# Kernel tuning notes

Hardware: AMD Instinct MI355X
Metric: run time of the kernel (lower is better)

The kernel has to match this reference:

```python
import jax, jax.numpy as jnp
import numpy as np

D = 1024   # feature_dim
K = 10     # num_anchors
B = 16384  # batch
H = 8      # num_heads


def setup_inputs() -> dict:
    key = jax.random.key(0)
    ks = jax.random.split(key, 12)
    f32 = jnp.float32

    def w(k, shape, scale=0.02):
        return (jax.random.normal(k, shape, f32) * scale)

    return {
        "features": jax.random.normal(ks[0], (B, D), f32),
        "anchors": w(ks[1], (K, D), 0.1),
        # anchor_refiner: Linear(D, D//2) -> ReLU -> Linear(D//2, D) -> Tanh
        "ar_w1": w(ks[2], (D, D // 2)), "ar_b1": jnp.zeros((D // 2,), f32),
        "ar_w2": w(ks[3], (D // 2, D)), "ar_b2": jnp.zeros((D,), f32),
        # attention projections
        "q_w": w(ks[4], (D, D)), "q_b": jnp.zeros((D,), f32),
        "k_w": w(ks[5], (D, D)), "k_b": jnp.zeros((D,), f32),
        "v_w": w(ks[6], (D, D)), "v_b": jnp.zeros((D,), f32),
        "o_w": w(ks[7], (D, D)), "o_b": jnp.zeros((D,), f32),
        # feature_enhancer: LayerNorm -> Linear(D,2D) -> GELU -> Linear(2D,D)
        "ln_g": jnp.ones((D,), f32), "ln_b": jnp.zeros((D,), f32),
        "ff_w1": w(ks[8], (D, 2 * D)), "ff_b1": jnp.zeros((2 * D,), f32),
        "ff_w2": w(ks[9], (2 * D, D)), "ff_b2": jnp.zeros((D,), f32),
        "div_w": jnp.asarray(0.001, f32),
        "cen_w": jnp.asarray(0.001, f32),
    }


def _l2norm(x, eps=1e-8):
    n = jnp.linalg.norm(x, axis=-1, keepdims=True)
    return x / jnp.maximum(n, eps)


def _layernorm(x, g, b, eps=1e-5):
    mu = jnp.mean(x, axis=-1, keepdims=True)
    var = jnp.mean(jnp.square(x - mu), axis=-1, keepdims=True)
    return (x - mu) * jax.lax.rsqrt(var + eps) * g + b


def reference(features, anchors, ar_w1, ar_b1, ar_w2, ar_b2,
              q_w, q_b, k_w, k_b, v_w, v_b, o_w, o_b,
              ln_g, ln_b, ff_w1, ff_b1, ff_w2, ff_b2, div_w, cen_w):
    b = features.shape[0]
    hd = D // H
    fn = _l2norm(features)                                 # [B, D]

    # anchor refinement
    refin = jnp.tanh(jax.nn.relu(anchors @ ar_w1 + ar_b1) @ ar_w2 + ar_b2)
    an = _l2norm(anchors + 0.1 * refin)                    # [K, D]

    # multi-head cross-attention to anchors
    q = (fn @ q_w + q_b).reshape(b, H, hd)                 # [B, H, hd]
    k = (an @ k_w + k_b).reshape(K, H, hd)                 # [K, H, hd]
    v = (an @ v_w + v_b).reshape(K, H, hd)
    scores = jnp.einsum('bhd,khd->bhk', q, k) / jnp.sqrt(jnp.asarray(hd, fn.dtype))
    aw = jax.nn.softmax(scores, axis=-1)                   # [B, H, K]
    att = jnp.einsum('bhk,khd->bhd', aw, v).reshape(b, D)
    att = att @ o_w + o_b

    # feature enhancer (dropout inactive: eval mode)
    enh = fn + 0.1 * att
    h = jax.nn.gelu(_layernorm(enh, ln_g, ln_b) @ ff_w1 + ff_b1, approximate=False)
    enh = h @ ff_w2 + ff_b2
    final = fn + 0.2 * enh                                 # [B, D]

    # diversity loss: pdist over K=10 anchors (45 pairs)
    diff = an[:, None, :] - an[None, :, :]                 # [K, K, D]
    dmat = jnp.sqrt(jnp.maximum(jnp.sum(diff * diff, -1), 1e-24))
    iu = np.triu_indices(K, 1)
    div_loss = jnp.exp(-jnp.maximum(dmat[iu].mean(), 1e-6))

    # center loss: attention-weighted feature-anchor distances
    avg_att = aw.mean(axis=1)                              # [B, K]
    sq = (jnp.sum(fn * fn, 1, keepdims=True) + jnp.sum(an * an, 1)
          - 2.0 * fn @ an.T)
    fa_dist = jnp.sqrt(jnp.maximum(sq, 1e-12))             # [B, K]
    center_loss = jnp.sum(avg_att * fa_dist, axis=1).mean()

    geo = jnp.abs(div_w) * div_loss + jnp.abs(cen_w) * center_loss
    geo = jnp.clip(geo, 0.0, 0.01)
    return final, geo
```

## Files before the change

kernel.cpp:

```cpp
#include <hip/hip_runtime.h>
#include <hip/hip_bf16.h>
#include <math.h>

typedef __hip_bfloat16 bf16;

#define D_  1024
#define K_  10
#define B_  16384
#define H_  8
#define HD_ 128

struct alignas(16) BF8 { bf16 v[8]; };
struct alignas(8)  BF4 { bf16 v[4]; };

typedef __bf16 bf8v __attribute__((ext_vector_type(8)));
typedef float  f4v  __attribute__((ext_vector_type(4)));

__device__ __forceinline__ float b2f(bf16 x){ return __bfloat162float(x); }
__device__ __forceinline__ bf16  f2b(float x){ return __float2bfloat16(x); }

#define GL2LDS16(g, l) __builtin_amdgcn_global_load_lds( \
    (__attribute__((address_space(1))) void*)(g), \
    (__attribute__((address_space(3))) void*)(l), 16, 0, 0)

__global__ __launch_bounds__(256) void l2norm_k(const float* __restrict__ x,
                                                bf16* __restrict__ fnb) {
  int b = blockIdx.x, t = threadIdx.x;
  float4 v = ((const float4*)(x + (size_t)b * D_))[t];
  float p = v.x*v.x + v.y*v.y + v.z*v.z + v.w*v.w;
  #pragma unroll
  for (int o = 32; o > 0; o >>= 1) p += __shfl_down(p, o);
  __shared__ float wsum[4];
  if ((t & 63) == 0) wsum[t >> 6] = p;
  __syncthreads();
  __shared__ float inv_s;
  if (t == 0) inv_s = 1.f / fmaxf(sqrtf(wsum[0]+wsum[1]+wsum[2]+wsum[3]), 1e-8f);
  __syncthreads();
  float iv = inv_s;
  BF4 o;
  o.v[0] = f2b(v.x*iv); o.v[1] = f2b(v.y*iv);
  o.v[2] = f2b(v.z*iv); o.v[3] = f2b(v.w*iv);
  ((BF4*)(fnb + (size_t)b * D_))[t] = o;
}

__global__ __launch_bounds__(256) void wt_k(const float* __restrict__ w,
                                            bf16* __restrict__ wt, int R, int C) {
  __shared__ float tle[32][33];
  int c0 = blockIdx.x * 32, r0 = blockIdx.y * 32;
  int tx = threadIdx.x & 31, ty = threadIdx.x >> 5;
  #pragma unroll
  for (int i = 0; i < 32; i += 8)
    tle[ty + i][tx] = w[(size_t)(r0 + ty + i) * C + c0 + tx];
  __syncthreads();
  #pragma unroll
  for (int i = 0; i < 32; i += 8)
    wt[(size_t)(c0 + ty + i) * R + r0 + tx] = f2b(tle[tx][ty + i]);
}

template<int COLS, int KD, int ACT>
__global__ __launch_bounds__(256) void panelmm_k(
    const float* __restrict__ A, const float* __restrict__ W,
    const float* __restrict__ bias, const float* __restrict__ aux,
    float* __restrict__ out,
    const float* __restrict__ W2, const float* __restrict__ bias2,
    float* __restrict__ out2, int N, int npanel) {
  constexpr int GROUPS = 256 / COLS;
  constexpr int DCH = KD / GROUPS;
  __shared__ float A_s[K_][KD];
  __shared__ float part[K_][COLS][GROUPS];
  const int t = threadIdx.x;
  int blk = blockIdx.x;
  const float* Wm = W; const float* bm = bias; float* om = out;
  if (blk >= npanel) { blk -= npanel; Wm = W2; bm = bias2; om = out2; }
  const int panel = blk;
  for (int i = t; i < K_*KD; i += 256) A_s[0][i] = A[i];
  __syncthreads();
  const int cg = t % COLS, g = t / COLS;
  const int col = panel*COLS + cg;
  float s[K_];
  #pragma unroll
  for (int r = 0; r < K_; ++r) s[r] = 0.f;
  const float* wp = Wm + (size_t)(g*DCH)*N + col;
  for (int d = g*DCH; d < (g+1)*DCH; ++d) {
    float wv = *wp; wp += N;
    #pragma unroll
    for (int r = 0; r < K_; ++r) s[r] = fmaf(A_s[r][d], wv, s[r]);
  }
  #pragma unroll
  for (int r = 0; r < K_; ++r) part[r][cg][g] = s[r];
  __syncthreads();
  for (int o = t; o < K_*COLS; o += 256) {
    int r = o / COLS, c = o % COLS;
    float v = 0.f;
    #pragma unroll
    for (int gg = 0; gg < GROUPS; ++gg) v += part[r][c][gg];
    v += bm[panel*COLS + c];
    if constexpr (ACT == 1) v = fmaxf(v, 0.f);
    if constexpr (ACT == 2) v = aux[(size_t)r*N + panel*COLS + c] + 0.1f*tanhf(v);
    om[(size_t)r*N + panel*COLS + c] = v;
  }
}

template<int TRANSOUT, typename TW>
__global__ __launch_bounds__(256) void smallmm_k(
    const float* __restrict__ A, const TW* __restrict__ W,
    bf16* __restrict__ outb, float scale) {
  constexpr int COLS = 64, GROUPS = 4, DCH = 32, NW = 1024;
  __shared__ float A_s[K_][128];
  __shared__ float part[K_][COLS][GROUPS];
  const int t = threadIdx.x;
  const int h = blockIdx.x & 7, panel = blockIdx.x >> 3;
  for (int i = t; i < K_*128; i += 256) {
    int r = i >> 7, j = i & 127;
    A_s[r][j] = A[r*1024 + h*128 + j];
  }
  __syncthreads();
  const int cg = t % COLS, g = t / COLS;
  const int col = panel*COLS + cg;
  float s[K_];
  #pragma unroll
  for (int r = 0; r < K_; ++r) s[r] = 0.f;
  const TW* wp = W + (size_t)(h*128 + g*DCH)*NW + col;
  for (int d = g*DCH; d < g*DCH + DCH; ++d) {
    float wv;
    if constexpr (sizeof(TW) == 2) wv = b2f(*wp); else wv = *wp;
    wp += NW;
    #pragma unroll
    for (int r = 0; r < K_; ++r) s[r] = fmaf(A_s[r][d], wv, s[r]);
  }
  #pragma unroll
  for (int r = 0; r < K_; ++r) part[r][cg][g] = s[r];
  __syncthreads();
  for (int o = t; o < 16*COLS; o += 256) {
    int r = o / COLS, c = o % COLS;
    float v = 0.f;
    if (r < K_) {
      #pragma unroll
      for (int gg = 0; gg < GROUPS; ++gg) v += part[r][c][gg];
      v *= scale;
    }
    if constexpr (TRANSOUT) outb[(size_t)(panel*COLS + c)*128 + h*16 + r] = f2b(v);
    else                    outb[(size_t)(h*16 + r)*NW + panel*COLS + c] = f2b(v);
  }
}

__global__ void sbias_k(const float* __restrict__ qb, const float* __restrict__ Km,
                        const float* __restrict__ na, float* __restrict__ sb) {
  int c = threadIdx.x;
  if (c < 128) {
    int h = c >> 4, k = c & 15;
    float s = 0.f;
    if (k < K_) {
      for (int j = 0; j < HD_; ++j)
        s = fmaf(qb[h*HD_ + j], Km[(size_t)k*D_ + h*HD_ + j], s);
    }
    sb[c] = s * 0.08838834764831845f;
  } else {
    int j = c - 128;
    sb[c] = (j < K_) ? (1.f + na[j]) : 0.f;
  }
}

__global__ __launch_bounds__(256) void anext_k(const float* __restrict__ an,
                                               bf16* __restrict__ wt) {
  int k = blockIdx.x;
  bf16* dst = wt + (size_t)(128 + k) * 1024;
  int i = threadIdx.x * 4;
  BF4 o;
  if (k < K_) {
    float4 a = *(const float4*)(an + (size_t)k*1024 + i);
    o.v[0] = f2b(-2.f*a.x); o.v[1] = f2b(-2.f*a.y);
    o.v[2] = f2b(-2.f*a.z); o.v[3] = f2b(-2.f*a.w);
  } else {
    o.v[0] = o.v[1] = o.v[2] = o.v[3] = f2b(0.f);
  }
  *(BF4*)(dst + i) = o;
}

__global__ __launch_bounds__(256) void ar3_k(const float* __restrict__ an_un,
    float* __restrict__ an, float* __restrict__ na, float* __restrict__ divloss) {
  __shared__ float a_s[K_][D_];
  __shared__ float nrm[K_];
  __shared__ float dm[45];
  const int t = threadIdx.x;
  for (int i = t; i < K_*D_; i += 256) a_s[0][i] = an_un[i];
  __syncthreads();
  const int wid = t >> 6, lane = t & 63;
  for (int r = wid; r < K_; r += 4) {
    float p = 0.f;
    for (int j = lane; j < D_; j += 64) p += a_s[r][j]*a_s[r][j];
    #pragma unroll
    for (int o = 1; o < 64; o <<= 1) p += __shfl_xor(p, o);
    if (lane == 0) nrm[r] = p;
  }
  __syncthreads();
  for (int i = t; i < K_*D_; i += 256) {
    int r = i >> 10;
    float iv = 1.f / fmaxf(sqrtf(nrm[r]), 1e-8f);
    float v = a_s[0][i] * iv;
    a_s[0][i] = v;
    an[i] = v;
  }
  if (t < K_) {
    float iv = 1.f / fmaxf(sqrtf(nrm[t]), 1e-8f);
    na[t] = nrm[t] * iv * iv;
  }
  __syncthreads();
  const int pr = t >> 2, sub = t & 3;
  if (pr < 45) {
    int i = 0, j = 0, c = pr;
    for (i = 0; i < K_; ++i) { int cnt = K_-1-i; if (c < cnt) { j = i+1+c; break; } c -= cnt; }
    float s = 0.f;
    for (int d = sub*256; d < sub*256 + 256; ++d) {
      float df = a_s[i][d] - a_s[j][d]; s += df*df;
    }
    s += __shfl_xor(s, 1); s += __shfl_xor(s, 2);
    if (sub == 0) dm[pr] = sqrtf(fmaxf(s, 1e-24f));
  }
  __syncthreads();
  if (t == 0) {
    float m = 0.f;
    for (int p = 0; p < 45; ++p) m += dm[p];
    m *= (1.f/45.f);
    *divloss = expf(-fmaxf(m, 1e-6f));
  }
}

template<int EPI, typename TO>
__global__ __launch_bounds__(256) void mgemm_k(
    const bf16* __restrict__ A, const bf16* __restrict__ Bt,
    const float* __restrict__ bias, const bf16* __restrict__ aux,
    TO* __restrict__ out, int M, int N, int Kd, float scale) {
  constexpr int BM = 128, BN = 128, BK = 32;
  __shared__ bf16 As[BM][BK];
  __shared__ bf16 Bs[BN][BK];
  const int tid = threadIdx.x;
  const int nMB = M / BM;
  const int nwg = gridDim.x;
  int wg = blockIdx.x;
  wg = (wg & 7) * (nwg >> 3) + (wg >> 3);
  const int mb = wg % nMB, nb = wg / nMB;
  const int bm = mb * BM, bn = nb * BN;

  const int srow = tid >> 2;
  const int sk   = (tid & 3) * 8;
  const bf16* ga = A  + (size_t)(bm + srow) * Kd + sk;
  const bf16* gb = Bt + (size_t)(bn + srow) * Kd + sk;
  const size_t rstep = (size_t)64 * Kd;
  bf16* la = &As[0][0] + tid * 8;
  bf16* lb = &Bs[0][0] + tid * 8;

  const int w    = tid >> 6;
  const int lane = tid & 63;
  const int wr = (w >> 1) * 64, wc = (w & 1) * 64;
  const int fr = lane & 15, fg = lane >> 4;

  f4v acc[4][4];
  const f4v zz = {0.f, 0.f, 0.f, 0.f};
  #pragma unroll
  for (int m = 0; m < 4; ++m)
    #pragma unroll
    for (int n = 0; n < 4; ++n) acc[m][n] = zz;

  for (int k0 = 0; k0 < Kd; k0 += BK) {
    GL2LDS16(ga,         la);
    GL2LDS16(ga + rstep, la + 2048);
    GL2LDS16(gb,         lb);
    GL2LDS16(gb + rstep, lb + 2048);
    __syncthreads();
    bf8v af[4], bf_[4];
    #pragma unroll
    for (int m = 0; m < 4; ++m)
      af[m] = *(const bf8v*)&As[wr + m*16 + fr][fg*8];
    #pragma unroll
    for (int n = 0; n < 4; ++n)
      bf_[n] = *(const bf8v*)&Bs[wc + n*16 + fr][fg*8];
    #pragma unroll
    for (int m = 0; m < 4; ++m)
      #pragma unroll
      for (int n = 0; n < 4; ++n)
        acc[m][n] = __builtin_amdgcn_mfma_f32_16x16x32_bf16(af[m], bf_[n], acc[m][n], 0, 0, 0);
    __syncthreads();
    ga += BK; gb += BK;
  }

  float bv[4];
  #pragma unroll
  for (int n = 0; n < 4; ++n) bv[n] = bias[bn + wc + n*16 + fr];
  #pragma unroll
  for (int m = 0; m < 4; ++m) {
    #pragma unroll
    for (int r = 0; r < 4; ++r) {
      const int row = bm + wr + m*16 + fg*4 + r;
      #pragma unroll
      for (int n = 0; n < 4; ++n) {
        const int col = bn + wc + n*16 + fr;
        float x = acc[m][n][r] + bv[n];
        if constexpr (EPI == 1) x = b2f(aux[(size_t)row * N + col]) + scale * x;
        if constexpr (EPI == 2) x = 0.5f * x * (1.f + erff(x * 0.70710678118654752f));
        if constexpr (sizeof(TO) == 2) out[(size_t)row * N + col] = f2b(x);
        else                           out[(size_t)row * N + col] = x;
      }
    }
  }
}

template<int EPI, typename TO>
__global__ __launch_bounds__(512) void mgemm256_k(
    const bf16* __restrict__ A, const bf16* __restrict__ Bt,
    const float* __restrict__ bias, const bf16* __restrict__ aux,
    TO* __restrict__ out, int M, int N, int Kd, float scale) {
  constexpr int BM = 256, BN = 256, BK = 64;
  __shared__ bf16 As[2][BM*BK];
  __shared__ bf16 Bs[2][BN*BK];
  const int tid = threadIdx.x;
  const int nMB = M / BM;
  const int nwg = gridDim.x;
  int wg = blockIdx.x;
  wg = (wg & 7) * (nwg >> 3) + (wg >> 3);
  const int bm = (wg % nMB) * BM, bn = (wg / nMB) * BN;

  const int srow = tid >> 3;
  const int scsw = ((tid & 7) ^ (srow & 7)) * 8;
  const bf16* gA = A  + (size_t)(bm + srow) * Kd + scsw;
  const bf16* gB = Bt + (size_t)(bn + srow) * Kd + scsw;
  const size_t lstep = (size_t)64 * Kd;

  const int wid = tid >> 6, lane = tid & 63;
  const int wm = wid >> 2, wn = wid & 3;
  const int fr = lane & 15, fg = lane >> 4;
  const int fsw = fr & 7;

  f4v acc[8][4];
  const f4v zz = {0.f, 0.f, 0.f, 0.f};
  #pragma unroll
  for (int m = 0; m < 8; ++m)
    #pragma unroll
    for (int n = 0; n < 4; ++n) acc[m][n] = zz;

  const int nt = Kd / BK;

  #pragma unroll
  for (int l = 0; l < 4; ++l) {
    GL2LDS16(gA + l*lstep, &As[0][0] + tid*8 + l*4096);
    GL2LDS16(gB + l*lstep, &Bs[0][0] + tid*8 + l*4096);
  }
  __syncthreads();

  int buf = 0;
  for (int t = 0; t < nt; ++t) {
    if (t + 1 < nt) {
      const int ko = (t + 1) * BK;
      #pragma unroll
      for (int l = 0; l < 4; ++l) {
        GL2LDS16(gA + l*lstep + ko, &As[buf^1][0] + tid*8 + l*4096);
        GL2LDS16(gB + l*lstep + ko, &Bs[buf^1][0] + tid*8 + l*4096);
      }
    }
    const bf16* la = &As[buf][0];
    const bf16* lb = &Bs[buf][0];
    bf8v bq[8];
    #pragma unroll
    for (int n = 0; n < 4; ++n) {
      const int rb = wn*64 + n*16 + fr;
      bq[n*2]   = *(const bf8v*)(lb + rb*64 + ((fg     ^ fsw) * 8));
      bq[n*2+1] = *(const bf8v*)(lb + rb*64 + (((4+fg) ^ fsw) * 8));
    }
    __builtin_amdgcn_s_setprio(1);
    #pragma unroll
    for (int m = 0; m < 8; ++m) {
      const int ra = wm*128 + m*16 + fr;
      bf8v a0 = *(const bf8v*)(la + ra*64 + ((fg     ^ fsw) * 8));
      bf8v a1 = *(const bf8v*)(la + ra*64 + (((4+fg) ^ fsw) * 8));
      #pragma unroll
      for (int n = 0; n < 4; ++n) {
        acc[m][n] = __builtin_amdgcn_mfma_f32_16x16x32_bf16(a0, bq[n*2],   acc[m][n], 0, 0, 0);
        acc[m][n] = __builtin_amdgcn_mfma_f32_16x16x32_bf16(a1, bq[n*2+1], acc[m][n], 0, 0, 0);
      }
    }
    __builtin_amdgcn_s_setprio(0);
    __syncthreads();
    buf ^= 1;
  }

  float bv[4];
  #pragma unroll
  for (int n = 0; n < 4; ++n) bv[n] = bias[bn + wn*64 + n*16 + fr];
  #pragma unroll
  for (int m = 0; m < 8; ++m) {
    #pragma unroll
    for (int r = 0; r < 4; ++r) {
      const int row = bm + wm*128 + m*16 + fg*4 + r;
      #pragma unroll
      for (int n = 0; n < 4; ++n) {
        const int col = bn + wn*64 + n*16 + fr;
        float x = acc[m][n][r] + bv[n];
        if constexpr (EPI == 1) x = b2f(aux[(size_t)row * N + col]) + scale * x;
        if constexpr (EPI == 2) x = 0.5f * x * (1.f + erff(x * 0.70710678118654752f));
        if constexpr (sizeof(TO) == 2) out[(size_t)row * N + col] = f2b(x);
        else                           out[(size_t)row * N + col] = x;
      }
    }
  }
}

__global__ __launch_bounds__(256) void attn2_k(
    const float* __restrict__ S, bf16* __restrict__ awp,
    float* __restrict__ cen_acc) {
  __shared__ float cred[4];
  const int t = threadIdx.x;
  const int wid = t >> 6, lane = t & 63;
  const int sub = lane & 7, head = lane >> 3;
  const int k0 = sub*2, k1 = k0 + 1;
  float c_acc = 0.f;
  const int row0 = blockIdx.x * 32 + wid * 8;

  for (int i = 0; i < 8; ++i) {
    const int row = row0 + i;
    const float* Sr = S + (size_t)row * 256;
    float2 sv = *(const float2*)(Sr + head*16 + k0);
    float v0 = (k0 < K_) ? sv.x : -1e30f;
    float v1 = (k1 < K_) ? sv.y : -1e30f;
    float m = fmaxf(v0, v1);
    m = fmaxf(m, __shfl_xor(m,1)); m = fmaxf(m, __shfl_xor(m,2)); m = fmaxf(m, __shfl_xor(m,4));
    float e0 = (k0 < K_) ? __expf(v0 - m) : 0.f;
    float e1 = (k1 < K_) ? __expf(v1 - m) : 0.f;
    float es = e0 + e1;
    es += __shfl_xor(es,1); es += __shfl_xor(es,2); es += __shfl_xor(es,4);
    float inv = 1.f / es;
    float a0 = e0 * inv, a1 = e1 * inv;
    bf16 b0 = f2b(a0), b1 = f2b(a1);
    unsigned int pk = (unsigned int)(*(unsigned short*)&b0)
                    | ((unsigned int)(*(unsigned short*)&b1) << 16);
    *(unsigned int*)(awp + (size_t)row*128 + head*16 + k0) = pk;
    float g0 = a0, g1 = a1;
    g0 += __shfl_xor(g0,8); g0 += __shfl_xor(g0,16); g0 += __shfl_xor(g0,32);
    g1 += __shfl_xor(g1,8); g1 += __shfl_xor(g1,16); g1 += __shfl_xor(g1,32);
    if (sub < 5) {
      float d20 = Sr[128 + k0];
      float d21 = Sr[128 + k1];
      c_acc = fmaf(g0, sqrtf(fmaxf(d20, 1e-12f)), c_acc);
      c_acc = fmaf(g1, sqrtf(fmaxf(d21, 1e-12f)), c_acc);
    }
  }
  #pragma unroll
  for (int o = 1; o < 64; o <<= 1) c_acc += __shfl_xor(c_acc, o);
  if (lane == 0) cred[wid] = c_acc;
  __syncthreads();
  if (t == 0) {
    float s = (cred[0]+cred[1]+cred[2]+cred[3]) * (1.f/64.f/(float)B_);
    atomicAdd(cen_acc, s);
  }
}

__global__ __launch_bounds__(256) void ln_k(const bf16* __restrict__ x,
    const float* __restrict__ g, const float* __restrict__ bta,
    bf16* __restrict__ out) {
  int b = blockIdx.x, t = threadIdx.x;
  BF4 ld = ((const BF4*)(x + (size_t)b * D_))[t];
  float v[4];
  #pragma unroll
  for (int j = 0; j < 4; ++j) v[j] = b2f(ld.v[j]);
  float s = v[0]+v[1]+v[2]+v[3];
  #pragma unroll
  for (int o = 32; o > 0; o >>= 1) s += __shfl_down(s, o);
  __shared__ float w1[4], w2[4];
  if ((t & 63) == 0) w1[t >> 6] = s;
  __syncthreads();
  __shared__ float mu_s, rs_s;
  if (t == 0) mu_s = (w1[0]+w1[1]+w1[2]+w1[3]) * (1.f/D_);
  __syncthreads();
  float mu = mu_s;
  float qv = 0.f;
  #pragma unroll
  for (int j = 0; j < 4; ++j) { float d = v[j]-mu; qv += d*d; }
  #pragma unroll
  for (int o = 32; o > 0; o >>= 1) qv += __shfl_down(qv, o);
  if ((t & 63) == 0) w2[t >> 6] = qv;
  __syncthreads();
  if (t == 0) rs_s = rsqrtf((w2[0]+w2[1]+w2[2]+w2[3]) * (1.f/D_) + 1e-5f);
  __syncthreads();
  float rs = rs_s;
  BF4 o;
  #pragma unroll
  for (int j = 0; j < 4; ++j) {
    int col = t*4 + j;
    o.v[j] = f2b((v[j]-mu)*rs*g[col] + bta[col]);
  }
  ((BF4*)(out + (size_t)b * D_))[t] = o;
}

__global__ void geo_k(const float* __restrict__ divl, const float* __restrict__ cen,
                      const float* __restrict__ div_w, const float* __restrict__ cen_w,
                      float* __restrict__ out) {
  float g = fabsf(*div_w) * (*divl) + fabsf(*cen_w) * (*cen);
  out[0] = fminf(fmaxf(g, 0.f), 0.01f);
}

extern "C" void kernel_launch(void* const* d_in, const int* in_sizes, int n_in,
                              void* d_out, int out_size, void* d_ws, size_t ws_size,
                              hipStream_t stream) {
  const float* features = (const float*)d_in[0];
  const float* anchors  = (const float*)d_in[1];
  const float* ar_w1 = (const float*)d_in[2];
  const float* ar_b1 = (const float*)d_in[3];
  const float* ar_w2 = (const float*)d_in[4];
  const float* ar_b2 = (const float*)d_in[5];
  const float* q_w = (const float*)d_in[6];
  const float* q_b = (const float*)d_in[7];
  const float* k_w = (const float*)d_in[8];
  const float* k_b = (const float*)d_in[9];
  const float* v_w = (const float*)d_in[10];
  const float* v_b = (const float*)d_in[11];
  const float* o_w = (const float*)d_in[12];
  const float* o_b = (const float*)d_in[13];
  const float* ln_g = (const float*)d_in[14];
  const float* ln_b = (const float*)d_in[15];
  const float* ff_w1 = (const float*)d_in[16];
  const float* ff_b1 = (const float*)d_in[17];
  const float* ff_w2 = (const float*)d_in[18];
  const float* ff_b2 = (const float*)d_in[19];
  const float* div_w = (const float*)d_in[20];
  const float* cen_w = (const float*)d_in[21];
  float* out = (float*)d_out;

  char* w = (char*)d_ws;
  bf16* ws_fnb = (bf16*)w;  w += (size_t)B_ * D_ * 2;
  bf16* ws_enh = (bf16*)w;  w += (size_t)B_ * D_ * 2;
  bf16* ws_ln  = (bf16*)w;  w += (size_t)B_ * D_ * 2;
  bf16* ws_h   = (bf16*)w;  w += (size_t)B_ * 2048 * 2;
  float* ws_S  = (float*)w; w += (size_t)B_ * 256 * 4;
  bf16* ws_awp = (bf16*)w;  w += (size_t)B_ * 128 * 2;
  bf16* ws_wq  = (bf16*)w;  w += (size_t)D_ * D_ * 2;
  bf16* ws_w1t = (bf16*)w;  w += (size_t)D_ * 2048 * 2;
  bf16* ws_w2t = (bf16*)w;  w += (size_t)2048 * D_ * 2;
  bf16* ws_wt  = (bf16*)w;  w += (size_t)256 * D_ * 2;
  bf16* ws_vt  = (bf16*)w;  w += (size_t)D_ * 128 * 2;
  float* ws_har = (float*)w;  w += (size_t)K_ * (D_/2) * 4;
  float* ws_anu = (float*)w;  w += (size_t)K_ * D_ * 4;
  float* ws_an  = (float*)w;  w += (size_t)K_ * D_ * 4;
  float* ws_k   = (float*)w;  w += (size_t)K_ * D_ * 4;
  float* ws_v   = (float*)w;  w += (size_t)K_ * D_ * 4;
  float* ws_na  = (float*)w;  w += 256;
  float* ws_div = (float*)w;  w += 256;
  float* ws_cen = (float*)w;  w += 256;
  float* ws_sb  = (float*)w;  w += 512;
  if ((size_t)(w - (char*)d_ws) > ws_size) return;

  hipMemsetAsync(ws_cen, 0, 4, stream);

  wt_k<<<dim3(D_/32,   D_/32),   256, 0, stream>>>(q_w,   ws_wq,  D_,   D_);
  wt_k<<<dim3(2048/32, D_/32),   256, 0, stream>>>(ff_w1, ws_w1t, D_,   2048);
  wt_k<<<dim3(D_/32,   2048/32), 256, 0, stream>>>(ff_w2, ws_w2t, 2048, D_);

  l2norm_k<<<B_, 256, 0, stream>>>(features, ws_fnb);

  panelmm_k<32, 1024, 1><<<16, 256, 0, stream>>>(
      anchors, ar_w1, ar_b1, nullptr, ws_har,
      nullptr, nullptr, nullptr, D_/2, 16);
  panelmm_k<64, 512, 2><<<16, 256, 0, stream>>>(
      ws_har, ar_w2, ar_b2, anchors, ws_anu,
      nullptr, nullptr, nullptr, D_, 16);
  ar3_k<<<1, 256, 0, stream>>>(ws_anu, ws_an, ws_na, ws_div);
  panelmm_k<64, 1024, 0><<<32, 256, 0, stream>>>(
      ws_an, k_w, k_b, nullptr, ws_k,
      v_w, v_b, ws_v, D_, 16);

  smallmm_k<0, bf16><<<128, 256, 0, stream>>>(ws_k, ws_wq, ws_wt, 0.08838834764831845f);
  anext_k<<<128, 256, 0, stream>>>(ws_an, ws_wt);
  sbias_k<<<1, 256, 0, stream>>>(q_b, ws_k, ws_na, ws_sb);
  smallmm_k<1, float><<<128, 256, 0, stream>>>(ws_v, o_w, ws_vt, 1.f);

  mgemm_k<0, float><<<dim3((B_/128)*(256/128)), 256, 0, stream>>>(
      ws_fnb, ws_wt, ws_sb, nullptr, ws_S, B_, 256, D_, 0.f);

  attn2_k<<<B_/32, 256, 0, stream>>>(ws_S, ws_awp, ws_cen);

  mgemm256_k<1, bf16><<<dim3((B_/256)*(D_/256)), 512, 0, stream>>>(
      ws_awp, ws_vt, o_b, ws_fnb, ws_enh, B_, D_, 128, 0.1f);

  ln_k<<<B_, 256, 0, stream>>>(ws_enh, ln_g, ln_b, ws_ln);

  mgemm256_k<2, bf16><<<dim3((B_/256)*(2048/256)), 512, 0, stream>>>(
      ws_ln, ws_w1t, ff_b1, nullptr, ws_h, B_, 2048, D_, 0.f);

  mgemm256_k<1, float><<<dim3((B_/256)*(D_/256)), 512, 0, stream>>>(
      ws_h, ws_w2t, ff_b2, ws_fnb, out, B_, D_, 2048, 0.2f);

  geo_k<<<1, 1, 0, stream>>>(ws_div, ws_cen, div_w, cen_w, out + (size_t)B_ * D_);
}
```

Baseline: 420.0 us.

## Double-buffer small GEMM, fuse prep/transpose launches, templatize K dims

Merges three weight-transpose launches into one kernel and four small prep kernels (K/V projection folding, anchor extension, score bias) into one multi-role kernel to cut launch overhead. Rewrites the 128x128 MFMA GEMM with double-buffered LDS, XOR-swizzled layout, and priority hints so global loads overlap compute. Makes K a compile-time template parameter for both GEMMs so loops can unroll. Switches the attention-output GEMM (K=128) from 256-tile to 128-tile to improve occupancy across CUs. These add code complexity and more LDS per block in the small GEMM.

```diff
diff --git a/kernel.cpp b/kernel.cpp
--- a/kernel.cpp
+++ b/kernel.cpp
@@ -43,10 +43,19 @@
   ((BF4*)(fnb + (size_t)b * D_))[t] = o;
 }
 
-__global__ __launch_bounds__(256) void wt_k(const float* __restrict__ w,
-                                            bf16* __restrict__ wt, int R, int C) {
+__global__ __launch_bounds__(256) void wt3_k(
+    const float* __restrict__ qw, const float* __restrict__ w1,
+    const float* __restrict__ w2,
+    bf16* __restrict__ o_qw, bf16* __restrict__ o_w1, bf16* __restrict__ o_w2) {
   __shared__ float tle[32][33];
-  int c0 = blockIdx.x * 32, r0 = blockIdx.y * 32;
+  int b = blockIdx.x;
+  const float* w; bf16* wt; int R, C, c0, r0;
+  if (b < 1024)      { w = qw; wt = o_qw; R = 1024; C = 1024;
+                       c0 = (b & 31) * 32;      r0 = (b >> 5) * 32; }
+  else if (b < 3072) { int i = b - 1024; w = w1; wt = o_w1; R = 1024; C = 2048;
+                       c0 = (i % 64) * 32;      r0 = (i / 64) * 32; }
+  else               { int i = b - 3072; w = w2; wt = o_w2; R = 2048; C = 1024;
+                       c0 = (i % 32) * 32;      r0 = (i / 32) * 32; }
   int tx = threadIdx.x & 31, ty = threadIdx.x >> 5;
   #pragma unroll
   for (int i = 0; i < 32; i += 8)
@@ -101,15 +110,63 @@
   }
 }
 
+__global__ __launch_bounds__(256) void ar3_k(const float* __restrict__ an_un,
+    float* __restrict__ an, float* __restrict__ na, float* __restrict__ divloss) {
+  __shared__ float a_s[K_][D_];
+  __shared__ float nrm[K_];
+  __shared__ float dm[45];
+  const int t = threadIdx.x;
+  for (int i = t; i < K_*D_; i += 256) a_s[0][i] = an_un[i];
+  __syncthreads();
+  const int wid = t >> 6, lane = t & 63;
+  for (int r = wid; r < K_; r += 4) {
+    float p = 0.f;
+    for (int j = lane; j < D_; j += 64) p += a_s[r][j]*a_s[r][j];
+    #pragma unroll
+    for (int o = 1; o < 64; o <<= 1) p += __shfl_xor(p, o);
+    if (lane == 0) nrm[r] = p;
+  }
+  __syncthreads();
+  for (int i = t; i < K_*D_; i += 256) {
+    int r = i >> 10;
+    float iv = 1.f / fmaxf(sqrtf(nrm[r]), 1e-8f);
+    float v = a_s[0][i] * iv;
+    a_s[0][i] = v;
+    an[i] = v;
+  }
+  if (t < K_) {
+    float iv = 1.f / fmaxf(sqrtf(nrm[t]), 1e-8f);
+    na[t] = nrm[t] * iv * iv;
+  }
+  __syncthreads();
+  const int pr = t >> 2, sub = t & 3;
+  if (pr < 45) {
+    int i = 0, j = 0, c = pr;
+    for (i = 0; i < K_; ++i) { int cnt = K_-1-i; if (c < cnt) { j = i+1+c; break; } c -= cnt; }
+    float s = 0.f;
+    for (int d = sub*256; d < sub*256 + 256; ++d) {
+      float df = a_s[i][d] - a_s[j][d]; s += df*df;
+    }
+    s += __shfl_xor(s, 1); s += __shfl_xor(s, 2);
+    if (sub == 0) dm[pr] = sqrtf(fmaxf(s, 1e-24f));
+  }
+  __syncthreads();
+  if (t == 0) {
+    float m = 0.f;
+    for (int p = 0; p < 45; ++p) m += dm[p];
+    m *= (1.f/45.f);
+    *divloss = expf(-fmaxf(m, 1e-6f));
+  }
+}
+
 template<int TRANSOUT, typename TW>
-__global__ __launch_bounds__(256) void smallmm_k(
-    const float* __restrict__ A, const TW* __restrict__ W,
-    bf16* __restrict__ outb, float scale) {
+__device__ __forceinline__ void smallmm_body(
+    int blk, const float* __restrict__ A, const TW* __restrict__ W,
+    bf16* __restrict__ outb, float scale,
+    float (&A_s)[K_][128], float (&part)[K_][64][4]) {
   constexpr int COLS = 64, GROUPS = 4, DCH = 32, NW = 1024;
-  __shared__ float A_s[K_][128];
-  __shared__ float part[K_][COLS][GROUPS];
   const int t = threadIdx.x;
-  const int h = blockIdx.x & 7, panel = blockIdx.x >> 3;
+  const int h = blk & 7, panel = blk >> 3;
   for (int i = t; i < K_*128; i += 256) {
     int r = i >> 7, j = i & 127;
     A_s[r][j] = A[r*1024 + h*128 + j];
@@ -121,12 +178,12 @@
   #pragma unroll
   for (int r = 0; r < K_; ++r) s[r] = 0.f;
   const TW* wp = W + (size_t)(h*128 + g*DCH)*NW + col;
-  for (int d = g*DCH; d < g*DCH + DCH; ++d) {
+  for (int d = 0; d < DCH; ++d) {
     float wv;
     if constexpr (sizeof(TW) == 2) wv = b2f(*wp); else wv = *wp;
     wp += NW;
     #pragma unroll
-    for (int r = 0; r < K_; ++r) s[r] = fmaf(A_s[r][d], wv, s[r]);
+    for (int r = 0; r < K_; ++r) s[r] = fmaf(A_s[r][g*DCH + d], wv, s[r]);
   }
   #pragma unroll
   for (int r = 0; r < K_; ++r) part[r][cg][g] = s[r];
@@ -144,116 +201,77 @@
   }
 }
 
-__global__ void sbias_k(const float* __restrict__ qb, const float* __restrict__ Km,
-                        const float* __restrict__ na, float* __restrict__ sb) {
-  int c = threadIdx.x;
-  if (c < 128) {
-    int h = c >> 4, k = c & 15;
-    float s = 0.f;
+__global__ __launch_bounds__(256) void prep_k(
+    const float* __restrict__ Km, const float* __restrict__ Vm,
+    const float* __restrict__ an, const float* __restrict__ na,
+    const bf16* __restrict__ wq, const float* __restrict__ ow,
+    const float* __restrict__ qb,
+    bf16* __restrict__ wt, bf16* __restrict__ vt, float* __restrict__ sb) {
+  __shared__ float A_s[K_][128];
+  __shared__ float part[K_][64][4];
+  const int b = blockIdx.x;
+  if (b < 128) {
+    smallmm_body<0, bf16>(b, Km, wq, wt, 0.08838834764831845f, A_s, part);
+  } else if (b < 256) {
+    smallmm_body<1, float>(b - 128, Vm, ow, vt, 1.f, A_s, part);
+  } else if (b < 384) {
+    int k = b - 256;
+    bf16* dst = wt + (size_t)(128 + k) * 1024;
+    int i = threadIdx.x * 4;
+    BF4 o;
     if (k < K_) {
-      for (int j = 0; j < HD_; ++j)
-        s = fmaf(qb[h*HD_ + j], Km[(size_t)k*D_ + h*HD_ + j], s);
-    }
-    sb[c] = s * 0.08838834764831845f;
+      float4 a = *(const float4*)(an + (size_t)k*1024 + i);
+      o.v[0] = f2b(-2.f*a.x); o.v[1] = f2b(-2.f*a.y);
+      o.v[2] = f2b(-2.f*a.z); o.v[3] = f2b(-2.f*a.w);
+    } else {
+      o.v[0] = o.v[1] = o.v[2] = o.v[3] = f2b(0.f);
+    }
+    *(BF4*)(dst + i) = o;
   } else {
-    int j = c - 128;
-    sb[c] = (j < K_) ? (1.f + na[j]) : 0.f;
-  }
-}
-
-__global__ __launch_bounds__(256) void anext_k(const float* __restrict__ an,
-                                               bf16* __restrict__ wt) {
-  int k = blockIdx.x;
-  bf16* dst = wt + (size_t)(128 + k) * 1024;
-  int i = threadIdx.x * 4;
-  BF4 o;
-  if (k < K_) {
-    float4 a = *(const float4*)(an + (size_t)k*1024 + i);
-    o.v[0] = f2b(-2.f*a.x); o.v[1] = f2b(-2.f*a.y);
-    o.v[2] = f2b(-2.f*a.z); o.v[3] = f2b(-2.f*a.w);
-  } else {
-    o.v[0] = o.v[1] = o.v[2] = o.v[3] = f2b(0.f);
-  }
-  *(BF4*)(dst + i) = o;
-}
-
-__global__ __launch_bounds__(256) void ar3_k(const float* __restrict__ an_un,
-    float* __restrict__ an, float* __restrict__ na, float* __restrict__ divloss) {
-  __shared__ float a_s[K_][D_];
-  __shared__ float nrm[K_];
-  __shared__ float dm[45];
-  const int t = threadIdx.x;
-  for (int i = t; i < K_*D_; i += 256) a_s[0][i] = an_un[i];
-  __syncthreads();
-  const int wid = t >> 6, lane = t & 63;
-  for (int r = wid; r < K_; r += 4) {
-    float p = 0.f;
-    for (int j = lane; j < D_; j += 64) p += a_s[r][j]*a_s[r][j];
-    #pragma unroll
-    for (int o = 1; o < 64; o <<= 1) p += __shfl_xor(p, o);
-    if (lane == 0) nrm[r] = p;
-  }
-  __syncthreads();
-  for (int i = t; i < K_*D_; i += 256) {
-    int r = i >> 10;
-    float iv = 1.f / fmaxf(sqrtf(nrm[r]), 1e-8f);
-    float v = a_s[0][i] * iv;
-    a_s[0][i] = v;
-    an[i] = v;
-  }
-  if (t < K_) {
-    float iv = 1.f / fmaxf(sqrtf(nrm[t]), 1e-8f);
-    na[t] = nrm[t] * iv * iv;
-  }
-  __syncthreads();
-  const int pr = t >> 2, sub = t & 3;
-  if (pr < 45) {
-    int i = 0, j = 0, c = pr;
-    for (i = 0; i < K_; ++i) { int cnt = K_-1-i; if (c < cnt) { j = i+1+c; break; } c -= cnt; }
-    float s = 0.f;
-    for (int d = sub*256; d < sub*256 + 256; ++d) {
-      float df = a_s[i][d] - a_s[j][d]; s += df*df;
-    }
-    s += __shfl_xor(s, 1); s += __shfl_xor(s, 2);
-    if (sub == 0) dm[pr] = sqrtf(fmaxf(s, 1e-24f));
-  }
-  __syncthreads();
-  if (t == 0) {
-    float m = 0.f;
-    for (int p = 0; p < 45; ++p) m += dm[p];
-    m *= (1.f/45.f);
-    *divloss = expf(-fmaxf(m, 1e-6f));
-  }
-}
-
-template<int EPI, typename TO>
+    int c = threadIdx.x;
+    if (c < 128) {
+      int h = c >> 4, k = c & 15;
+      float s = 0.f;
+      if (k < K_) {
+        for (int j = 0; j < HD_; ++j)
+          s = fmaf(qb[h*HD_ + j], Km[(size_t)k*D_ + h*HD_ + j], s);
+      }
+      sb[c] = s * 0.08838834764831845f;
+    } else {
+      int j = c - 128;
+      sb[c] = (j < K_) ? (1.f + na[j]) : 0.f;
+    }
+  }
+}
+
+template<int EPI, int KD, typename TO>
 __global__ __launch_bounds__(256) void mgemm_k(
     const bf16* __restrict__ A, const bf16* __restrict__ Bt,
     const float* __restrict__ bias, const bf16* __restrict__ aux,
-    TO* __restrict__ out, int M, int N, int Kd, float scale) {
+    TO* __restrict__ out, int M, int N, float scale) {
   constexpr int BM = 128, BN = 128, BK = 32;
-  __shared__ bf16 As[BM][BK];
-  __shared__ bf16 Bs[BN][BK];
+  constexpr int nt = KD / BK;
+  __shared__ bf16 As[2][BM*BK];
+  __shared__ bf16 Bs[2][BN*BK];
   const int tid = threadIdx.x;
   const int nMB = M / BM;
   const int nwg = gridDim.x;
   int wg = blockIdx.x;
   wg = (wg & 7) * (nwg >> 3) + (wg >> 3);
-  const int mb = wg % nMB, nb = wg / nMB;
-  const int bm = mb * BM, bn = nb * BN;
+  const int bm = (wg % nMB) * BM, bn = (wg / nMB) * BN;
 
   const int srow = tid >> 2;
-  const int sk   = (tid & 3) * 8;
-  const bf16* ga = A  + (size_t)(bm + srow) * Kd + sk;
-  const bf16* gb = Bt + (size_t)(bn + srow) * Kd + sk;
-  const size_t rstep = (size_t)64 * Kd;
-  bf16* la = &As[0][0] + tid * 8;
-  bf16* lb = &Bs[0][0] + tid * 8;
+  const int ssw  = (((tid & 3) ^ ((tid >> 3) & 3)) * 8);
+  const bf16* gA = A  + (size_t)(bm + srow) * KD + ssw;
+  const bf16* gB = Bt + (size_t)(bn + srow) * KD + ssw;
+  const size_t rstep = (size_t)64 * KD;
 
   const int w    = tid >> 6;
   const int lane = tid & 63;
   const int wr = (w >> 1) * 64, wc = (w & 1) * 64;
   const int fr = lane & 15, fg = lane >> 4;
+  const int key = (fr >> 1) & 3;
+  const int co  = (fg ^ key) * 8;
 
   f4v acc[4][4];
   const f4v zz = {0.f, 0.f, 0.f, 0.f};
@@ -262,26 +280,39 @@
     #pragma unroll
     for (int n = 0; n < 4; ++n) acc[m][n] = zz;
 
-  for (int k0 = 0; k0 < Kd; k0 += BK) {
-    GL2LDS16(ga,         la);
-    GL2LDS16(ga + rstep, la + 2048);
-    GL2LDS16(gb,         lb);
-    GL2LDS16(gb + rstep, lb + 2048);
-    __syncthreads();
-    bf8v af[4], bf_[4];
+  GL2LDS16(gA,         &As[0][0] + tid*8);
+  GL2LDS16(gA + rstep, &As[0][0] + tid*8 + 2048);
+  GL2LDS16(gB,         &Bs[0][0] + tid*8);
+  GL2LDS16(gB + rstep, &Bs[0][0] + tid*8 + 2048);
+  __syncthreads();
+
+  #pragma unroll 2
+  for (int t = 0; t < nt; ++t) {
+    const int buf = t & 1;
+    if (t + 1 < nt) {
+      const int ko = (t + 1) * BK;
+      GL2LDS16(gA + ko,         &As[buf^1][0] + tid*8);
+      GL2LDS16(gA + rstep + ko, &As[buf^1][0] + tid*8 + 2048);
+      GL2LDS16(gB + ko,         &Bs[buf^1][0] + tid*8);
+      GL2LDS16(gB + rstep + ko, &Bs[buf^1][0] + tid*8 + 2048);
+    }
+    const bf16* la = &As[buf][0];
+    const bf16* lb = &Bs[buf][0];
+    bf8v af[4], bq[4];
     #pragma unroll
     for (int m = 0; m < 4; ++m)
-      af[m] = *(const bf8v*)&As[wr + m*16 + fr][fg*8];
+      af[m] = *(const bf8v*)(la + (wr + m*16 + fr)*BK + co);
     #pragma unroll
     for (int n = 0; n < 4; ++n)
-      bf_[n] = *(const bf8v*)&Bs[wc + n*16 + fr][fg*8];
+      bq[n] = *(const bf8v*)(lb + (wc + n*16 + fr)*BK + co);
+    __builtin_amdgcn_s_setprio(1);
     #pragma unroll
     for (int m = 0; m < 4; ++m)
       #pragma unroll
       for (int n = 0; n < 4; ++n)
-        acc[m][n] = __builtin_amdgcn_mfma_f32_16x16x32_bf16(af[m], bf_[n], acc[m][n], 0, 0, 0);
+        acc[m][n] = __builtin_amdgcn_mfma_f32_16x16x32_bf16(af[m], bq[n], acc[m][n], 0, 0, 0);
+    __builtin_amdgcn_s_setprio(0);
     __syncthreads();
-    ga += BK; gb += BK;
   }
 
   float bv[4];
@@ -305,12 +336,13 @@
   }
 }
 
-template<int EPI, typename TO>
+template<int EPI, int KD, typename TO>
 __global__ __launch_bounds__(512) void mgemm256_k(
     const bf16* __restrict__ A, const bf16* __restrict__ Bt,
     const float* __restrict__ bias, const bf16* __restrict__ aux,
-    TO* __restrict__ out, int M, int N, int Kd, float scale) {
+    TO* __restrict__ out, int M, int N, float scale) {
   constexpr int BM = 256, BN = 256, BK = 64;
+  constexpr int nt = KD / BK;
   __shared__ bf16 As[2][BM*BK];
   __shared__ bf16 Bs[2][BN*BK];
   const int tid = threadIdx.x;
@@ -322,14 +354,16 @@
 
   const int srow = tid >> 3;
   const int scsw = ((tid & 7) ^ (srow & 7)) * 8;
-  const bf16* gA = A  + (size_t)(bm + srow) * Kd + scsw;
-  const bf16* gB = Bt + (size_t)(bn + srow) * Kd + scsw;
-  const size_t lstep = (size_t)64 * Kd;
+  const bf16* gA = A  + (size_t)(bm + srow) * KD + scsw;
+  const bf16* gB = Bt + (size_t)(bn + srow) * KD + scsw;
+  const size_t lstep = (size_t)64 * KD;
 
   const int wid = tid >> 6, lane = tid & 63;
   const int wm = wid >> 2, wn = wid & 3;
   const int fr = lane & 15, fg = lane >> 4;
   const int fsw = fr & 7;
+  const int c0 = ((fg     ^ fsw) * 8);
+  const int c1 = (((4+fg) ^ fsw) * 8);
 
   f4v acc[8][4];
   const f4v zz = {0.f, 0.f, 0.f, 0.f};
@@ -337,8 +371,6 @@
   for (int m = 0; m < 8; ++m)
     #pragma unroll
     for (int n = 0; n < 4; ++n) acc[m][n] = zz;
-
-  const int nt = Kd / BK;
 
   #pragma unroll
   for (int l = 0; l < 4; ++l) {
@@ -347,8 +379,9 @@
   }
   __syncthreads();
 
-  int buf = 0;
+  #pragma unroll 2
   for (int t = 0; t < nt; ++t) {
+    const int buf = t & 1;
     if (t + 1 < nt) {
       const int ko = (t + 1) * BK;
       #pragma unroll
@@ -363,15 +396,15 @@
     #pragma unroll
     for (int n = 0; n < 4; ++n) {
       const int rb = wn*64 + n*16 + fr;
-      bq[n*2]   = *(const bf8v*)(lb + rb*64 + ((fg     ^ fsw) * 8));
-      bq[n*2+1] = *(const bf8v*)(lb + rb*64 + (((4+fg) ^ fsw) * 8));
+      bq[n*2]   = *(const bf8v*)(lb + rb*64 + c0);
+      bq[n*2+1] = *(const bf8v*)(lb + rb*64 + c1);
     }
     __builtin_amdgcn_s_setprio(1);
     #pragma unroll
     for (int m = 0; m < 8; ++m) {
       const int ra = wm*128 + m*16 + fr;
-      bf8v a0 = *(const bf8v*)(la + ra*64 + ((fg     ^ fsw) * 8));
-      bf8v a1 = *(const bf8v*)(la + ra*64 + (((4+fg) ^ fsw) * 8));
+      bf8v a0 = *(const bf8v*)(la + ra*64 + c0);
+      bf8v a1 = *(const bf8v*)(la + ra*64 + c1);
       #pragma unroll
       for (int n = 0; n < 4; ++n) {
         acc[m][n] = __builtin_amdgcn_mfma_f32_16x16x32_bf16(a0, bq[n*2],   acc[m][n], 0, 0, 0);
@@ -380,7 +413,6 @@
     }
     __builtin_amdgcn_s_setprio(0);
     __syncthreads();
-    buf ^= 1;
   }
 
   float bv[4];
@@ -549,9 +581,7 @@
 
   hipMemsetAsync(ws_cen, 0, 4, stream);
 
-  wt_k<<<dim3(D_/32,   D_/32),   256, 0, stream>>>(q_w,   ws_wq,  D_,   D_);
-  wt_k<<<dim3(2048/32, D_/32),   256, 0, stream>>>(ff_w1, ws_w1t, D_,   2048);
-  wt_k<<<dim3(D_/32,   2048/32), 256, 0, stream>>>(ff_w2, ws_w2t, 2048, D_);
+  wt3_k<<<5120, 256, 0, stream>>>(q_w, ff_w1, ff_w2, ws_wq, ws_w1t, ws_w2t);
 
   l2norm_k<<<B_, 256, 0, stream>>>(features, ws_fnb);
 
@@ -566,26 +596,24 @@
       ws_an, k_w, k_b, nullptr, ws_k,
       v_w, v_b, ws_v, D_, 16);
 
-  smallmm_k<0, bf16><<<128, 256, 0, stream>>>(ws_k, ws_wq, ws_wt, 0.08838834764831845f);
-  anext_k<<<128, 256, 0, stream>>>(ws_an, ws_wt);
-  sbias_k<<<1, 256, 0, stream>>>(q_b, ws_k, ws_na, ws_sb);
-  smallmm_k<1, float><<<128, 256, 0, stream>>>(ws_v, o_w, ws_vt, 1.f);
-
-  mgemm_k<0, float><<<dim3((B_/128)*(256/128)), 256, 0, stream>>>(
-      ws_fnb, ws_wt, ws_sb, nullptr, ws_S, B_, 256, D_, 0.f);
+  prep_k<<<385, 256, 0, stream>>>(ws_k, ws_v, ws_an, ws_na,
+                                  ws_wq, o_w, q_b, ws_wt, ws_vt, ws_sb);
+
+  mgemm_k<0, 1024, float><<<dim3((B_/128)*(256/128)), 256, 0, stream>>>(
+      ws_fnb, ws_wt, ws_sb, nullptr, ws_S, B_, 256, 0.f);
 
   attn2_k<<<B_/32, 256, 0, stream>>>(ws_S, ws_awp, ws_cen);
 
-  mgemm256_k<1, bf16><<<dim3((B_/256)*(D_/256)), 512, 0, stream>>>(
-      ws_awp, ws_vt, o_b, ws_fnb, ws_enh, B_, D_, 128, 0.1f);
+  mgemm_k<1, 128, bf16><<<dim3((B_/128)*(D_/128)), 256, 0, stream>>>(
+      ws_awp, ws_vt, o_b, ws_fnb, ws_enh, B_, D_, 0.1f);
 
   ln_k<<<B_, 256, 0, stream>>>(ws_enh, ln_g, ln_b, ws_ln);
 
-  mgemm256_k<2, bf16><<<dim3((B_/256)*(2048/256)), 512, 0, stream>>>(
-      ws_ln, ws_w1t, ff_b1, nullptr, ws_h, B_, 2048, D_, 0.f);
-
-  mgemm256_k<1, float><<<dim3((B_/256)*(D_/256)), 512, 0, stream>>>(
-      ws_h, ws_w2t, ff_b2, ws_fnb, out, B_, D_, 2048, 0.2f);
+  mgemm256_k<2, 1024, bf16><<<dim3((B_/256)*(2048/256)), 512, 0, stream>>>(
+      ws_ln, ws_w1t, ff_b1, nullptr, ws_h, B_, 2048, 0.f);
+
+  mgemm256_k<1, 2048, float><<<dim3((B_/256)*(D_/256)), 512, 0, stream>>>(
+      ws_h, ws_w2t, ff_b2, ws_fnb, out, B_, D_, 0.2f);
 
   geo_k<<<1, 1, 0, stream>>>(ws_div, ws_cen, div_w, cen_w, out + (size_t)B_ * D_);
 }
```

New measurement: 399.7 us. -4.8%, faster.
